# Optimization experiments

Measured on AMD Instinct MI355X. Metric: run time of the kernel, lower is better.

## Reference

```python
import jax, jax.numpy as jnp
import numpy as np

EPS_SK = 1e-8   # Sinkhorn epsilon
EPS_LN = 1e-5   # torch LayerNorm default eps
N_ITER = 20


def _layer_norm(x, eps=EPS_LN):
    mu = jnp.mean(x, axis=-1, keepdims=True)
    var = jnp.mean((x - mu) ** 2, axis=-1, keepdims=True)
    return (x - mu) * jax.lax.rsqrt(var + eps)


def _sinkhorn(H):
    M = jnp.exp(H)
    def body(_, M):
        M = M / (jnp.sum(M, axis=-1, keepdims=True) + EPS_SK)
        M = M / (jnp.sum(M, axis=-2, keepdims=True) + EPS_SK)
        return M
    return jax.lax.fori_loop(0, N_ITER, body, M)


def setup_inputs() -> dict:
    key = jax.random.key(0)
    ks = jax.random.split(key, 12)
    B, S, D = 8192, 4, 1024
    sc_in = 1.0 / np.sqrt(S * D)
    sc_d = 1.0 / np.sqrt(D)
    return {
        "x": jax.random.normal(ks[0], (B, D), jnp.float32),
        "x_streams": jax.random.normal(ks[1], (B, S, D), jnp.float32),
        "W_pre": jax.random.normal(ks[2], (S, S * D), jnp.float32) * sc_in,
        "b_pre": jnp.zeros((S,), jnp.float32),
        "W_post": jax.random.normal(ks[3], (S, S * D), jnp.float32) * sc_in,
        "b_post": jnp.zeros((S,), jnp.float32),
        "W_res": jax.random.normal(ks[4], (S * S, S * D), jnp.float32) * sc_in,
        "b_res": jnp.zeros((S * S,), jnp.float32),
        "alpha_pre": jnp.float32(0.01),
        "alpha_post": jnp.float32(0.01),
        "alpha_res": jnp.float32(0.01),
        "gamma": jnp.ones((D,), jnp.float32),
        "beta": jnp.zeros((D,), jnp.float32),
        "W_layer": jax.random.normal(ks[5], (D, D), jnp.float32) * sc_d,
        "b_layer": jnp.zeros((D,), jnp.float32),
    }


def reference(x, x_streams, W_pre, b_pre, W_post, b_post, W_res, b_res,
              alpha_pre, alpha_post, alpha_res, gamma, beta, W_layer, b_layer):
    B = x.shape[0]
    S = x_streams.shape[1]
    x_flat = x_streams.reshape(B, -1)            # [B, S*D]
    x_norm = _layer_norm(x_flat)                 # F.layer_norm, no affine

    h_pre = jax.nn.sigmoid(alpha_pre * (x_norm @ W_pre.T + b_pre))   # [B, S]
    x_agg = jnp.einsum('bs,bsd->bd', h_pre, x_streams)               # [B, D]

    # layer_fn modeled as a Linear (self.norm has affine gamma/beta)
    out = (_layer_norm(x_agg) * gamma + beta) @ W_layer.T + b_layer  # [B, D]

    h_post = 2.0 * jax.nn.sigmoid(alpha_post * (x_norm @ W_post.T + b_post))  # [B, S]
    h_res_logits = alpha_res * (x_norm @ W_res.T + b_res)                      # [B, S*S]
    h_res = _sinkhorn(h_res_logits.reshape(B, S, S))                           # [B, S, S]

    mixed = jnp.einsum('bst,btd->bsd', h_res, x_streams)             # [B, S, D]
    updated = mixed + out[:, None, :] * h_post[:, :, None]
    return (jnp.mean(updated, axis=1), updated)
```

## Files before the change

kernel.cpp:

```cpp
#include <hip/hip_runtime.h>

#define DEV __device__ __forceinline__

typedef __bf16 bf16x8 __attribute__((ext_vector_type(8)));
typedef float f32x4 __attribute__((ext_vector_type(4)));
typedef unsigned int u32;

constexpr int BROWS = 8192;
constexpr int D = 1024;
constexpr int SD = 4096;

DEV unsigned short f2bf(float f) {
  unsigned int u = __float_as_uint(f);
  u = (u + 0x7FFFu + ((u >> 16) & 1u)) >> 16;
  return (unsigned short)u;
}

DEV float wred(float v) {
#pragma unroll
  for (int m = 1; m < 64; m <<= 1) v += __shfl_xor(v, m);
  return v;
}

DEV float sigmoidf(float x) { return 1.0f / (1.0f + __expf(-x)); }

DEV void async_ld16(const void* g, void* l) {
  __builtin_amdgcn_global_load_lds((const __attribute__((address_space(1))) u32*)g,
                                   (__attribute__((address_space(3))) u32*)l, 16, 0, 0);
}

__global__ __launch_bounds__(256) void k0_wsum(
    const float* __restrict__ Wpre, const float* __restrict__ Wpost,
    const float* __restrict__ Wres, float* __restrict__ wsum) {
  const int j = blockIdx.x;
  const float* src = (j < 4) ? (Wpre + j * SD)
                             : (j < 8 ? (Wpost + (j - 4) * SD) : (Wres + (j - 8) * SD));
  float s = 0.f;
  for (int i = threadIdx.x * 4; i < SD; i += 1024) {
    float4 v = *(const float4*)(src + i);
    s += v.x + v.y + v.z + v.w;
  }
  s = wred(s);
  __shared__ float tmp[4];
  if ((threadIdx.x & 63) == 0) tmp[threadIdx.x >> 6] = s;
  __syncthreads();
  if (threadIdx.x == 0) wsum[j] = tmp[0] + tmp[1] + tmp[2] + tmp[3];
}

__global__ __launch_bounds__(256) void k0_conv(const float* __restrict__ W,
                                               unsigned short* __restrict__ out) {
  const int i = (blockIdx.x * 256 + threadIdx.x) * 4;
  float4 v = *(const float4*)(W + i);
  ushort4 u;
  u.x = f2bf(v.x); u.y = f2bf(v.y); u.z = f2bf(v.z); u.w = f2bf(v.w);
  *(ushort4*)(out + i) = u;
}

__global__ __launch_bounds__(256) void k1_rowpass(
    const float* __restrict__ xs,
    const float* __restrict__ Wpre, const float* __restrict__ bpre,
    const float* __restrict__ Wpost, const float* __restrict__ bpost,
    const float* __restrict__ Wres, const float* __restrict__ bres,
    const float* __restrict__ s_apre, const float* __restrict__ s_apost,
    const float* __restrict__ s_ares,
    const float* __restrict__ gamma, const float* __restrict__ beta,
    const float* __restrict__ wsum,
    unsigned short* __restrict__ lnagg,
    float* __restrict__ hres_g, float* __restrict__ hpost_g) {
  const int tid = threadIdx.x;
  const int wv = tid >> 6;
  const int ln = tid & 63;
  const int rb = blockIdx.x * 4;

  __shared__ float DOT[24][4];
  __shared__ float HPRE[4][4];

  const int jb = wv * 6;
  const float* Wj[6];
#pragma unroll
  for (int q = 0; q < 6; ++q) {
    const int j = jb + q;
    Wj[q] = (j < 4) ? (Wpre + j * SD) : (j < 8) ? (Wpost + (j - 4) * SD) : (Wres + (j - 8) * SD);
  }
  const float* xr0 = xs + (size_t)(rb + 0) * SD;
  const float* xr1 = xs + (size_t)(rb + 1) * SD;
  const float* xr2 = xs + (size_t)(rb + 2) * SD;
  const float* xr3 = xs + (size_t)(rb + 3) * SD;

  float acc6[6][4];
#pragma unroll
  for (int q = 0; q < 6; ++q)
#pragma unroll
    for (int r = 0; r < 4; ++r) acc6[q][r] = 0.f;
  float sum4[4] = {0.f, 0.f, 0.f, 0.f}, sq4[4] = {0.f, 0.f, 0.f, 0.f};

#pragma unroll 1
  for (int it = 0; it < 16; ++it) {
    const int i = it * 256 + ln * 4;
    float4 xv[4];
    xv[0] = *(const float4*)(xr0 + i);
    xv[1] = *(const float4*)(xr1 + i);
    xv[2] = *(const float4*)(xr2 + i);
    xv[3] = *(const float4*)(xr3 + i);
#pragma unroll
    for (int r = 0; r < 4; ++r) {
      sum4[r] += xv[r].x + xv[r].y + xv[r].z + xv[r].w;
      sq4[r] += xv[r].x * xv[r].x + xv[r].y * xv[r].y + xv[r].z * xv[r].z + xv[r].w * xv[r].w;
    }
#pragma unroll
    for (int q = 0; q < 6; ++q) {
      const float4 w = *(const float4*)(Wj[q] + i);
#pragma unroll
      for (int r = 0; r < 4; ++r)
        acc6[q][r] += w.x * xv[r].x + w.y * xv[r].y + w.z * xv[r].z + w.w * xv[r].w;
    }
  }

#pragma unroll
  for (int q = 0; q < 6; ++q)
#pragma unroll
    for (int r = 0; r < 4; ++r) acc6[q][r] = wred(acc6[q][r]);
#pragma unroll
  for (int r = 0; r < 4; ++r) { sum4[r] = wred(sum4[r]); sq4[r] = wred(sq4[r]); }

  float mu4[4], rs4[4];
#pragma unroll
  for (int r = 0; r < 4; ++r) {
    mu4[r] = sum4[r] * (1.0f / 4096.0f);
    rs4[r] = rsqrtf(sq4[r] * (1.0f / 4096.0f) - mu4[r] * mu4[r] + 1e-5f);
  }

  if (ln == 0) {
#pragma unroll
    for (int q = 0; q < 6; ++q)
#pragma unroll
      for (int r = 0; r < 4; ++r) DOT[jb + q][r] = acc6[q][r];
  }
  __syncthreads();

  if (wv == 0) {
    const float ares = s_ares[0];
    const int rr = ln >> 4, jj = ln & 15;
    const float corr = rs4[rr] * (DOT[8 + jj][rr] - mu4[rr] * wsum[8 + jj]);
    float M = __expf(ares * (corr + bres[jj]));
#pragma unroll 1
    for (int itr = 0; itr < 20; ++itr) {
      float rs = M + __shfl_xor(M, 1);
      rs += __shfl_xor(rs, 2);
      M *= __builtin_amdgcn_rcpf(rs + 1e-8f);
      float cs = M + __shfl_xor(M, 4);
      cs += __shfl_xor(cs, 8);
      M *= __builtin_amdgcn_rcpf(cs + 1e-8f);
    }
    hres_g[(size_t)rb * 16 + ln] = M;
  } else if (wv == 1) {
    if (ln < 16) {
      const int r = ln >> 2, s = ln & 3;
      const float corr = rs4[r] * (DOT[s][r] - mu4[r] * wsum[s]);
      HPRE[r][s] = sigmoidf(s_apre[0] * (corr + bpre[s]));
    } else if (ln < 32) {
      const int idx = ln - 16, r = idx >> 2, s = idx & 3;
      const float corr = rs4[r] * (DOT[4 + s][r] - mu4[r] * wsum[4 + s]);
      hpost_g[(rb + r) * 4 + s] = 2.0f * sigmoidf(s_apost[0] * (corr + bpost[s]));
    }
  }
  __syncthreads();

  {
    const int b = rb + wv;
    const float* xb = xs + (size_t)b * SD;
    const float h0 = HPRE[wv][0], h1 = HPRE[wv][1], h2 = HPRE[wv][2], h3 = HPRE[wv][3];
    float4 agg[4];
    float asum = 0.f, asq = 0.f;
#pragma unroll
    for (int i2 = 0; i2 < 4; ++i2) {
      const int d = i2 * 256 + ln * 4;
      float4 g0 = *(const float4*)(xb + d);
      float4 g1 = *(const float4*)(xb + D + d);
      float4 g2 = *(const float4*)(xb + 2 * D + d);
      float4 g3 = *(const float4*)(xb + 3 * D + d);
      float4 a;
      a.x = h0 * g0.x + h1 * g1.x + h2 * g2.x + h3 * g3.x;
      a.y = h0 * g0.y + h1 * g1.y + h2 * g2.y + h3 * g3.y;
      a.z = h0 * g0.z + h1 * g1.z + h2 * g2.z + h3 * g3.z;
      a.w = h0 * g0.w + h1 * g1.w + h2 * g2.w + h3 * g3.w;
      agg[i2] = a;
      asum += a.x + a.y + a.z + a.w;
      asq += a.x * a.x + a.y * a.y + a.z * a.z + a.w * a.w;
    }
    asum = wred(asum);
    asq = wred(asq);
    const float mu2 = asum * (1.0f / 1024.0f);
    const float rstd2 = rsqrtf(asq * (1.0f / 1024.0f) - mu2 * mu2 + 1e-5f);
#pragma unroll
    for (int i2 = 0; i2 < 4; ++i2) {
      const int d = i2 * 256 + ln * 4;
      float4 g = *(const float4*)(gamma + d);
      float4 bb = *(const float4*)(beta + d);
      ushort4 u;
      u.x = f2bf((agg[i2].x - mu2) * rstd2 * g.x + bb.x);
      u.y = f2bf((agg[i2].y - mu2) * rstd2 * g.y + bb.y);
      u.z = f2bf((agg[i2].z - mu2) * rstd2 * g.z + bb.z);
      u.w = f2bf((agg[i2].w - mu2) * rstd2 * g.w + bb.w);
      *(ushort4*)(lnagg + (size_t)b * D + d) = u;
    }
  }
}

__global__ __launch_bounds__(256) void k2_gemm_ep(
    const unsigned short* __restrict__ A,
    const unsigned short* __restrict__ Bw,
    const float* __restrict__ blayer,
    const float* __restrict__ xs,
    const float* __restrict__ hres_g, const float* __restrict__ hpost_g,
    float* __restrict__ outMean, float* __restrict__ outUpd) {
  __shared__ char smem[44032];
  char* AsB = smem;
  char* BsB = smem + 16384;
  float* EP = (float*)smem;
  float* HR = (float*)(smem + 32768);
  float* HP = (float*)(smem + 41472);

  const int tid = threadIdx.x;
  const int l = tid & 63;
  const int wv = tid >> 6;
  const int wm = wv >> 1, wn = wv & 1;
  const int lrow = l & 15, lq = l >> 4;
  const int bm0 = blockIdx.x * 128;
  const int bn0 = blockIdx.y * 128;

#pragma unroll
  for (int i = 0; i < 8; ++i) {
    int idx = i * 256 + tid;
    HR[(idx >> 4) * 17 + (idx & 15)] = hres_g[(size_t)bm0 * 16 + idx];
  }
#pragma unroll
  for (int i = 0; i < 2; ++i) {
    int idx = i * 256 + tid;
    HP[(idx >> 2) * 5 + (idx & 3)] = hpost_g[(size_t)bm0 * 4 + idx];
  }

  f32x4 acc[4][4] = {};

#pragma unroll 1
  for (int kt = 0; kt < 16; ++kt) {
    __syncthreads();
#pragma unroll
    for (int c = 0; c < 4; ++c) {
      const int idx = c * 256 + tid;
      const int row = idx >> 3, cc = idx & 7;
      const int gch = cc ^ (row & 7);
      async_ld16((const char*)A + ((size_t)(bm0 + row) << 11) + kt * 128 + gch * 16,
                 AsB + idx * 16);
      async_ld16((const char*)Bw + ((size_t)(bn0 + row) << 11) + kt * 128 + gch * 16,
                 BsB + idx * 16);
    }
    __syncthreads();
#pragma unroll
    for (int kk = 0; kk < 2; ++kk) {
      bf16x8 af[4], bfr[4];
      const int sw = (kk * 4 + lq);
#pragma unroll
      for (int t = 0; t < 4; ++t) {
        const int ra = wm * 64 + t * 16 + lrow;
        const int rbr = wn * 64 + t * 16 + lrow;
        af[t] = *(const bf16x8*)(AsB + ra * 128 + (sw ^ (ra & 7)) * 16);
        bfr[t] = *(const bf16x8*)(BsB + rbr * 128 + (sw ^ (rbr & 7)) * 16);
      }
#pragma unroll
      for (int ti = 0; ti < 4; ++ti)
#pragma unroll
        for (int tj = 0; tj < 4; ++tj)
          acc[ti][tj] =
              __builtin_amdgcn_mfma_f32_16x16x32_bf16(af[ti], bfr[tj], acc[ti][tj], 0, 0, 0);
    }
  }

#pragma unroll
  for (int ti = 0; ti < 4; ++ti) {
    __syncthreads();
#pragma unroll
    for (int tj = 0; tj < 4; ++tj)
#pragma unroll
      for (int r2 = 0; r2 < 4; ++r2)
        EP[(wm * 16 + lq * 4 + r2) * 132 + wn * 64 + tj * 16 + lrow] = acc[ti][tj][r2];
    __syncthreads();

    const int rr2 = tid >> 3;
    const int c0 = (tid & 7) * 4;
    const int bl = (rr2 >> 4) * 64 + ti * 16 + (rr2 & 15);
    const int gr = bm0 + bl;
    float hr[16], hp4[4];
#pragma unroll
    for (int q = 0; q < 16; ++q) hr[q] = HR[bl * 17 + q];
#pragma unroll
    for (int q = 0; q < 4; ++q) hp4[q] = HP[bl * 5 + q];
    const float cm0 = 0.25f * (hr[0] + hr[4] + hr[8] + hr[12]);
    const float cm1 = 0.25f * (hr[1] + hr[5] + hr[9] + hr[13]);
    const float cm2 = 0.25f * (hr[2] + hr[6] + hr[10] + hr[14]);
    const float cm3 = 0.25f * (hr[3] + hr[7] + hr[11] + hr[15]);
    const float hps = 0.25f * (hp4[0] + hp4[1] + hp4[2] + hp4[3]);
    const float* xb = xs + (size_t)gr * SD + bn0;
    float* um = outMean + (size_t)gr * 1024 + bn0;
    float* uu = outUpd + (size_t)gr * 4096 + bn0;
#pragma unroll
    for (int k2i = 0; k2i < 4; ++k2i) {
      const int col = c0 + k2i * 32;
      f32x4 ov = *(const f32x4*)(EP + rr2 * 132 + col);
      ov += *(const f32x4*)(blayer + bn0 + col);
      const f32x4 x0 = *(const f32x4*)(xb + col);
      const f32x4 x1 = *(const f32x4*)(xb + 1024 + col);
      const f32x4 x2 = *(const f32x4*)(xb + 2048 + col);
      const f32x4 x3 = *(const f32x4*)(xb + 3072 + col);
      *(f32x4*)(um + col) = cm0 * x0 + cm1 * x1 + cm2 * x2 + cm3 * x3 + ov * hps;
      *(f32x4*)(uu + col) = hr[0] * x0 + hr[1] * x1 + hr[2] * x2 + hr[3] * x3 + ov * hp4[0];
      *(f32x4*)(uu + 1024 + col) = hr[4] * x0 + hr[5] * x1 + hr[6] * x2 + hr[7] * x3 + ov * hp4[1];
      *(f32x4*)(uu + 2048 + col) = hr[8] * x0 + hr[9] * x1 + hr[10] * x2 + hr[11] * x3 + ov * hp4[2];
      *(f32x4*)(uu + 3072 + col) = hr[12] * x0 + hr[13] * x1 + hr[14] * x2 + hr[15] * x3 + ov * hp4[3];
    }
  }
}

extern "C" void kernel_launch(void* const* d_in, const int* in_sizes, int n_in,
                              void* d_out, int out_size, void* d_ws, size_t ws_size,
                              hipStream_t stream) {
  const float* xs = (const float*)d_in[1];
  const float* Wpre = (const float*)d_in[2];
  const float* bpre = (const float*)d_in[3];
  const float* Wpost = (const float*)d_in[4];
  const float* bpost = (const float*)d_in[5];
  const float* Wres = (const float*)d_in[6];
  const float* bres = (const float*)d_in[7];
  const float* apre = (const float*)d_in[8];
  const float* apost = (const float*)d_in[9];
  const float* ares = (const float*)d_in[10];
  const float* gamma = (const float*)d_in[11];
  const float* beta = (const float*)d_in[12];
  const float* Wlayer = (const float*)d_in[13];
  const float* blayer = (const float*)d_in[14];

  const size_t OFF_LNAGG = (size_t)2 << 20;
  const size_t OFF_HRES = (size_t)18 << 20;
  const size_t OFF_HPOST = OFF_HRES + (size_t)BROWS * 16 * 4;
  const size_t OFF_WSUM = OFF_HPOST + (size_t)BROWS * 4 * 4;
  if (ws_size < OFF_WSUM + 128) return;

  char* ws = (char*)d_ws;
  unsigned short* wl16 = (unsigned short*)ws;
  unsigned short* lnagg = (unsigned short*)(ws + OFF_LNAGG);
  float* hresb = (float*)(ws + OFF_HRES);
  float* hpostb = (float*)(ws + OFF_HPOST);
  float* wsum = (float*)(ws + OFF_WSUM);

  float* outMean = (float*)d_out;
  float* outUpd = outMean + (size_t)BROWS * D;

  hipLaunchKernelGGL(k0_wsum, dim3(24), dim3(256), 0, stream, Wpre, Wpost, Wres, wsum);
  hipLaunchKernelGGL(k0_conv, dim3(1024), dim3(256), 0, stream, Wlayer, wl16);
  hipLaunchKernelGGL(k1_rowpass, dim3(2048), dim3(256), 0, stream, xs, Wpre, bpre, Wpost,
                     bpost, Wres, bres, apre, apost, ares, gamma, beta, wsum, lnagg, hresb,
                     hpostb);
  hipLaunchKernelGGL(k2_gemm_ep, dim3(64, 8), dim3(256), 0, stream, lnagg, wl16, blayer, xs,
                     hresb, hpostb, outMean, outUpd);
}
```

Before: 408.6 us.

## Fuse prep kernels, pack projection weights, double-buffer rowpass loads, nontemporal stores

Merges the weight-sum and bf16 conversion kernels into one launch, which also copies the 24 projection weight rows into a contiguous workspace buffer so the row pass can address them with one base pointer. The row-pass reduction loop is software-pipelined with two register buffers so loads for the next slice are issued before the current slice is computed. The epilogue's output writes become nontemporal stores to avoid polluting cache with write-once data. The changes cost extra registers in the row pass and an extra weight copy.

```diff
diff --git a/kernel.cpp b/kernel.cpp
--- a/kernel.cpp
+++ b/kernel.cpp
@@ -29,38 +29,39 @@
                                    (__attribute__((address_space(3))) u32*)l, 16, 0, 0);
 }
 
-__global__ __launch_bounds__(256) void k0_wsum(
-    const float* __restrict__ Wpre, const float* __restrict__ Wpost,
-    const float* __restrict__ Wres, float* __restrict__ wsum) {
-  const int j = blockIdx.x;
-  const float* src = (j < 4) ? (Wpre + j * SD)
-                             : (j < 8 ? (Wpost + (j - 4) * SD) : (Wres + (j - 8) * SD));
-  float s = 0.f;
-  for (int i = threadIdx.x * 4; i < SD; i += 1024) {
-    float4 v = *(const float4*)(src + i);
-    s += v.x + v.y + v.z + v.w;
-  }
-  s = wred(s);
-  __shared__ float tmp[4];
-  if ((threadIdx.x & 63) == 0) tmp[threadIdx.x >> 6] = s;
-  __syncthreads();
-  if (threadIdx.x == 0) wsum[j] = tmp[0] + tmp[1] + tmp[2] + tmp[3];
-}
-
-__global__ __launch_bounds__(256) void k0_conv(const float* __restrict__ W,
-                                               unsigned short* __restrict__ out) {
-  const int i = (blockIdx.x * 256 + threadIdx.x) * 4;
-  float4 v = *(const float4*)(W + i);
-  ushort4 u;
-  u.x = f2bf(v.x); u.y = f2bf(v.y); u.z = f2bf(v.z); u.w = f2bf(v.w);
-  *(ushort4*)(out + i) = u;
+__global__ __launch_bounds__(256) void k0_prep(
+    const float* __restrict__ Wlayer, const float* __restrict__ Wpre,
+    const float* __restrict__ Wpost, const float* __restrict__ Wres,
+    unsigned short* __restrict__ wl16, float* __restrict__ Wall,
+    float* __restrict__ wsum) {
+  const int bx = blockIdx.x, tid = threadIdx.x;
+  if (bx < 1024) {
+    const int i = bx * 1024 + tid * 4;
+    float4 v = *(const float4*)(Wlayer + i);
+    ushort4 u = make_ushort4(f2bf(v.x), f2bf(v.y), f2bf(v.z), f2bf(v.w));
+    *(ushort4*)(wl16 + i) = u;
+  } else {
+    const int j = bx - 1024;
+    const float* src = (j < 4) ? (Wpre + j * SD)
+                               : (j < 8 ? (Wpost + (j - 4) * SD) : (Wres + (j - 8) * SD));
+    float s = 0.f;
+    for (int i = tid * 4; i < SD; i += 1024) {
+      float4 v = *(const float4*)(src + i);
+      *(float4*)(Wall + j * SD + i) = v;
+      s += v.x + v.y + v.z + v.w;
+    }
+    s = wred(s);
+    __shared__ float tmp[4];
+    if ((tid & 63) == 0) tmp[tid >> 6] = s;
+    __syncthreads();
+    if (tid == 0) wsum[j] = tmp[0] + tmp[1] + tmp[2] + tmp[3];
+  }
 }
 
 __global__ __launch_bounds__(256) void k1_rowpass(
-    const float* __restrict__ xs,
-    const float* __restrict__ Wpre, const float* __restrict__ bpre,
-    const float* __restrict__ Wpost, const float* __restrict__ bpost,
-    const float* __restrict__ Wres, const float* __restrict__ bres,
+    const float* __restrict__ xs, const float* __restrict__ Wall,
+    const float* __restrict__ bpre, const float* __restrict__ bpost,
+    const float* __restrict__ bres,
     const float* __restrict__ s_apre, const float* __restrict__ s_apost,
     const float* __restrict__ s_ares,
     const float* __restrict__ gamma, const float* __restrict__ beta,
@@ -76,16 +77,9 @@
   __shared__ float HPRE[4][4];
 
   const int jb = wv * 6;
-  const float* Wj[6];
-#pragma unroll
-  for (int q = 0; q < 6; ++q) {
-    const int j = jb + q;
-    Wj[q] = (j < 4) ? (Wpre + j * SD) : (j < 8) ? (Wpost + (j - 4) * SD) : (Wres + (j - 8) * SD);
-  }
-  const float* xr0 = xs + (size_t)(rb + 0) * SD;
-  const float* xr1 = xs + (size_t)(rb + 1) * SD;
-  const float* xr2 = xs + (size_t)(rb + 2) * SD;
-  const float* xr3 = xs + (size_t)(rb + 3) * SD;
+  const float* Wb = Wall + (size_t)jb * SD;
+  const float* xb0 = xs + (size_t)rb * SD;
+  const int l4 = ln * 4;
 
   float acc6[6][4];
 #pragma unroll
@@ -94,27 +88,51 @@
     for (int r = 0; r < 4; ++r) acc6[q][r] = 0.f;
   float sum4[4] = {0.f, 0.f, 0.f, 0.f}, sq4[4] = {0.f, 0.f, 0.f, 0.f};
 
+  float4 xA[4], wA[6], xB[4], wB[6];
+
+#define LDX(dst, it)                                      \
+  {                                                       \
+    const int i_ = (it)*256 + l4;                         \
+    dst[0] = *(const float4*)(xb0 + i_);                  \
+    dst[1] = *(const float4*)(xb0 + SD + i_);             \
+    dst[2] = *(const float4*)(xb0 + 2 * SD + i_);         \
+    dst[3] = *(const float4*)(xb0 + 3 * SD + i_);         \
+  }
+#define LDW(dst, it)                                      \
+  {                                                       \
+    const int i_ = (it)*256 + l4;                         \
+    _Pragma("unroll") for (int q = 0; q < 6; ++q)         \
+        dst[q] = *(const float4*)(Wb + q * SD + i_);      \
+  }
+#define CMP(X, W)                                                              \
+  {                                                                            \
+    _Pragma("unroll") for (int r = 0; r < 4; ++r) {                            \
+      sum4[r] += X[r].x + X[r].y + X[r].z + X[r].w;                            \
+      sq4[r] += X[r].x * X[r].x + X[r].y * X[r].y + X[r].z * X[r].z +          \
+                X[r].w * X[r].w;                                               \
+    }                                                                          \
+    _Pragma("unroll") for (int q = 0; q < 6; ++q) {                            \
+      _Pragma("unroll") for (int r = 0; r < 4; ++r) acc6[q][r] +=              \
+          W[q].x * X[r].x + W[q].y * X[r].y + W[q].z * X[r].z + W[q].w * X[r].w;\
+    }                                                                          \
+  }
+
+  LDX(xA, 0);
+  LDW(wA, 0);
 #pragma unroll 1
-  for (int it = 0; it < 16; ++it) {
-    const int i = it * 256 + ln * 4;
-    float4 xv[4];
-    xv[0] = *(const float4*)(xr0 + i);
-    xv[1] = *(const float4*)(xr1 + i);
-    xv[2] = *(const float4*)(xr2 + i);
-    xv[3] = *(const float4*)(xr3 + i);
-#pragma unroll
-    for (int r = 0; r < 4; ++r) {
-      sum4[r] += xv[r].x + xv[r].y + xv[r].z + xv[r].w;
-      sq4[r] += xv[r].x * xv[r].x + xv[r].y * xv[r].y + xv[r].z * xv[r].z + xv[r].w * xv[r].w;
-    }
-#pragma unroll
-    for (int q = 0; q < 6; ++q) {
-      const float4 w = *(const float4*)(Wj[q] + i);
-#pragma unroll
-      for (int r = 0; r < 4; ++r)
-        acc6[q][r] += w.x * xv[r].x + w.y * xv[r].y + w.z * xv[r].z + w.w * xv[r].w;
-    }
-  }
+  for (int it = 0; it < 16; it += 2) {
+    LDX(xB, it + 1);
+    LDW(wB, it + 1);
+    CMP(xA, wA);
+    if (it < 14) {
+      LDX(xA, it + 2);
+      LDW(wA, it + 2);
+    }
+    CMP(xB, wB);
+  }
+#undef LDX
+#undef LDW
+#undef CMP
 
 #pragma unroll
   for (int q = 0; q < 6; ++q)
@@ -174,7 +192,7 @@
     float asum = 0.f, asq = 0.f;
 #pragma unroll
     for (int i2 = 0; i2 < 4; ++i2) {
-      const int d = i2 * 256 + ln * 4;
+      const int d = i2 * 256 + l4;
       float4 g0 = *(const float4*)(xb + d);
       float4 g1 = *(const float4*)(xb + D + d);
       float4 g2 = *(const float4*)(xb + 2 * D + d);
@@ -194,7 +212,7 @@
     const float rstd2 = rsqrtf(asq * (1.0f / 1024.0f) - mu2 * mu2 + 1e-5f);
 #pragma unroll
     for (int i2 = 0; i2 < 4; ++i2) {
-      const int d = i2 * 256 + ln * 4;
+      const int d = i2 * 256 + l4;
       float4 g = *(const float4*)(gamma + d);
       float4 bb = *(const float4*)(beta + d);
       ushort4 u;
@@ -312,11 +330,16 @@
       const f32x4 x1 = *(const f32x4*)(xb + 1024 + col);
       const f32x4 x2 = *(const f32x4*)(xb + 2048 + col);
       const f32x4 x3 = *(const f32x4*)(xb + 3072 + col);
-      *(f32x4*)(um + col) = cm0 * x0 + cm1 * x1 + cm2 * x2 + cm3 * x3 + ov * hps;
-      *(f32x4*)(uu + col) = hr[0] * x0 + hr[1] * x1 + hr[2] * x2 + hr[3] * x3 + ov * hp4[0];
-      *(f32x4*)(uu + 1024 + col) = hr[4] * x0 + hr[5] * x1 + hr[6] * x2 + hr[7] * x3 + ov * hp4[1];
-      *(f32x4*)(uu + 2048 + col) = hr[8] * x0 + hr[9] * x1 + hr[10] * x2 + hr[11] * x3 + ov * hp4[2];
-      *(f32x4*)(uu + 3072 + col) = hr[12] * x0 + hr[13] * x1 + hr[14] * x2 + hr[15] * x3 + ov * hp4[3];
+      __builtin_nontemporal_store(cm0 * x0 + cm1 * x1 + cm2 * x2 + cm3 * x3 + ov * hps,
+                                  (f32x4*)(um + col));
+      __builtin_nontemporal_store(hr[0] * x0 + hr[1] * x1 + hr[2] * x2 + hr[3] * x3 + ov * hp4[0],
+                                  (f32x4*)(uu + col));
+      __builtin_nontemporal_store(hr[4] * x0 + hr[5] * x1 + hr[6] * x2 + hr[7] * x3 + ov * hp4[1],
+                                  (f32x4*)(uu + 1024 + col));
+      __builtin_nontemporal_store(hr[8] * x0 + hr[9] * x1 + hr[10] * x2 + hr[11] * x3 + ov * hp4[2],
+                                  (f32x4*)(uu + 2048 + col));
+      __builtin_nontemporal_store(hr[12] * x0 + hr[13] * x1 + hr[14] * x2 + hr[15] * x3 + ov * hp4[3],
+                                  (f32x4*)(uu + 3072 + col));
     }
   }
 }
@@ -343,7 +366,9 @@
   const size_t OFF_HRES = (size_t)18 << 20;
   const size_t OFF_HPOST = OFF_HRES + (size_t)BROWS * 16 * 4;
   const size_t OFF_WSUM = OFF_HPOST + (size_t)BROWS * 4 * 4;
-  if (ws_size < OFF_WSUM + 128) return;
+  const size_t OFF_WALL = OFF_WSUM + 512;
+  const size_t NEED = OFF_WALL + (size_t)24 * SD * 4;
+  if (ws_size < NEED) return;
 
   char* ws = (char*)d_ws;
   unsigned short* wl16 = (unsigned short*)ws;
@@ -351,15 +376,15 @@
   float* hresb = (float*)(ws + OFF_HRES);
   float* hpostb = (float*)(ws + OFF_HPOST);
   float* wsum = (float*)(ws + OFF_WSUM);
+  float* Wall = (float*)(ws + OFF_WALL);
 
   float* outMean = (float*)d_out;
   float* outUpd = outMean + (size_t)BROWS * D;
 
-  hipLaunchKernelGGL(k0_wsum, dim3(24), dim3(256), 0, stream, Wpre, Wpost, Wres, wsum);
-  hipLaunchKernelGGL(k0_conv, dim3(1024), dim3(256), 0, stream, Wlayer, wl16);
-  hipLaunchKernelGGL(k1_rowpass, dim3(2048), dim3(256), 0, stream, xs, Wpre, bpre, Wpost,
-                     bpost, Wres, bres, apre, apost, ares, gamma, beta, wsum, lnagg, hresb,
-                     hpostb);
+  hipLaunchKernelGGL(k0_prep, dim3(1048), dim3(256), 0, stream, Wlayer, Wpre, Wpost, Wres,
+                     wl16, Wall, wsum);
+  hipLaunchKernelGGL(k1_rowpass, dim3(2048), dim3(256), 0, stream, xs, Wall, bpre, bpost,
+                     bres, apre, apost, ares, gamma, beta, wsum, lnagg, hresb, hpostb);
   hipLaunchKernelGGL(k2_gemm_ep, dim3(64, 8), dim3(256), 0, stream, lnagg, wl16, blayer, xs,
                      hresb, hpostb, outMean, outUpd);
 }
```

Result: faster. 396.2 us (-3.0%).
